# Optimization experiments

Measured on AMD Instinct MI355X. Metric: run time of the kernel, lower is better.

## Reference

```python
import jax, jax.numpy as jnp
import numpy as np

NUM_HEADS = 16

def setup_inputs() -> dict:
    key = jax.random.key(0)
    ks = jax.random.split(key, 6)
    B, S, D = 4, 2048, 1024
    sc = 1.0 / np.sqrt(D)
    return {
        "x": jax.random.normal(ks[0], (B, S, D), jnp.float32),
        "Wq": jax.random.normal(ks[1], (D, D), jnp.float32) * sc,
        "Wk": jax.random.normal(ks[2], (D, D), jnp.float32) * sc,
        "Wv": jax.random.normal(ks[3], (D, D), jnp.float32) * sc,
        "Wo": jax.random.normal(ks[4], (D, D), jnp.float32) * sc,
        "bo": jnp.zeros((D,), jnp.float32),
    }

def reference(x, Wq, Wk, Wv, Wo, bo):
    B, S, D = x.shape
    H = NUM_HEADS
    hd = D // H
    # projections (Linear: x @ W^T, but we store W as [d_in, d_out] so x @ W)
    q = (x @ Wq).reshape(B, S, H, hd)
    k = (x @ Wk).reshape(B, S, H, hd)
    v = (x @ Wv).reshape(B, S, H, hd)
    # scores: [B, H, S, S]
    scores = jnp.einsum("bqhd,bkhd->bhqk", q, k) / jnp.sqrt(jnp.asarray(hd, x.dtype))
    attn = jax.nn.softmax(scores, axis=-1)  # dropout p=0.0 (eval) -> identity
    ctx = jnp.einsum("bhqk,bkhd->bqhd", attn, v).reshape(B, S, D)
    return ctx @ Wo + bo
```

## Files before the change

kernel.cpp:

```cpp
#include <hip/hip_runtime.h>
#include <hip/hip_bf16.h>

typedef __bf16 bf16x8 __attribute__((ext_vector_type(8)));
typedef float f32x4 __attribute__((ext_vector_type(4)));

#define D_MODEL 1024
#define SEQ 2048
#define BATCH 4
#define HEADS 16
#define HD 64
#define M_TOT (BATCH * SEQ)
#define QPW 4

static __device__ __forceinline__ unsigned short f2bf(float f) {
  unsigned int u = __float_as_uint(f);
  unsigned int lsb = (u >> 16) & 1u;
  u += 0x7fffu + lsb;
  return (unsigned short)(u >> 16);
}

static __device__ __forceinline__ void glds16(const void* g, void* l) {
  __builtin_amdgcn_global_load_lds(
      (const __attribute__((address_space(1))) unsigned int*)g,
      (__attribute__((address_space(3))) unsigned int*)l, 16, 0, 0);
}

__global__ __launch_bounds__(256) void cvt_x_kernel(const float* __restrict__ x,
                                                    unsigned short* __restrict__ xb,
                                                    int n4) {
  int i = blockIdx.x * 256 + threadIdx.x;
  if (i >= n4) return;
  const float4 v = reinterpret_cast<const float4*>(x)[i];
  ushort4 o;
  o.x = f2bf(v.x); o.y = f2bf(v.y); o.z = f2bf(v.z); o.w = f2bf(v.w);
  reinterpret_cast<ushort4*>(xb)[i] = o;
}

__global__ __launch_bounds__(256) void transW_kernel(const float* __restrict__ W,
                                                     unsigned short* __restrict__ Wt) {
  __shared__ float t[32][33];
  int bx = blockIdx.x * 32;
  int by = blockIdx.y * 32;
  int tx = threadIdx.x, ty = threadIdx.y;
#pragma unroll
  for (int i = 0; i < 32; i += 8)
    t[ty + i][tx] = W[(size_t)(by + ty + i) * D_MODEL + bx + tx];
  __syncthreads();
#pragma unroll
  for (int i = 0; i < 32; i += 8)
    Wt[(size_t)(bx + ty + i) * D_MODEL + by + tx] = f2bf(t[tx][ty + i]);
}

template <int MODE>
__global__ __launch_bounds__(256) void gemm_bt_kernel(
    const unsigned short* __restrict__ A, const unsigned short* __restrict__ Bt,
    void* __restrict__ out, const float* __restrict__ bias, int M, int N, int K,
    float scale) {
  __shared__ __align__(16) unsigned short Als[128 * 64];
  __shared__ __align__(16) unsigned short Bls[128 * 64];

  const int tid = threadIdx.x;
  const int l = tid & 63;
  const int wave = tid >> 6;
  const int l15 = l & 15;
  const int lk = l >> 4;
  const int wm = wave >> 1, wn = wave & 1;

  const int nblocks_n = N >> 7;
  const int mblk = blockIdx.x / nblocks_n;
  const int nblk = blockIdx.x % nblocks_n;
  const int m0 = mblk << 7, n0 = nblk << 7;

  f32x4 acc[4][4] = {};

  const int srow0 = wave * 32 + (l >> 3);
  const int scolb = (l & 7) * 16;
  char* alsb = (char*)Als;
  char* blsb = (char*)Bls;

  for (int k0 = 0; k0 < K; k0 += 64) {
    __syncthreads();
#pragma unroll
    for (int j = 0; j < 4; ++j) {
      const int row = srow0 + j * 8;
      glds16((const char*)A + ((size_t)(m0 + row) * K + k0) * 2 + scolb,
             alsb + (wave * 32 + j * 8) * 128);
      glds16((const char*)Bt + ((size_t)(n0 + row) * K + k0) * 2 + scolb,
             blsb + (wave * 32 + j * 8) * 128);
    }
    __syncthreads();
#pragma unroll
    for (int kk = 0; kk < 2; ++kk) {
      bf16x8 af[4], bfr[4];
#pragma unroll
      for (int m = 0; m < 4; ++m)
        af[m] = *reinterpret_cast<const bf16x8*>(
            alsb + (wm * 64 + m * 16 + l15) * 128 + kk * 64 + lk * 16);
#pragma unroll
      for (int n = 0; n < 4; ++n)
        bfr[n] = *reinterpret_cast<const bf16x8*>(
            blsb + (wn * 64 + n * 16 + l15) * 128 + kk * 64 + lk * 16);
#pragma unroll
      for (int m = 0; m < 4; ++m)
#pragma unroll
        for (int n = 0; n < 4; ++n)
          acc[m][n] = __builtin_amdgcn_mfma_f32_16x16x32_bf16(af[m], bfr[n], acc[m][n], 0, 0, 0);
    }
  }

#pragma unroll
  for (int m = 0; m < 4; ++m) {
#pragma unroll
    for (int n = 0; n < 4; ++n) {
      const int row0 = wm * 64 + m * 16 + lk * 4;
      const int col = wn * 64 + n * 16 + l15;
      const int gm0 = m0 + row0;
      const int gn = n0 + col;
      if (MODE == 0) {
        unsigned short* o = (unsigned short*)out;
#pragma unroll
        for (int r = 0; r < 4; ++r)
          o[(size_t)(gm0 + r) * N + gn] = f2bf(acc[m][n][r] * scale);
      } else if (MODE == 1) {
        unsigned short* o = (unsigned short*)out;
        int b = gm0 >> 11, s = gm0 & 2047;
        int h = gn >> 6, d = gn & 63;
        size_t base = ((size_t)((b * HEADS + h) * HD + d)) * SEQ + s;
#pragma unroll
        for (int r = 0; r < 4; ++r) o[base + r] = f2bf(acc[m][n][r]);
      } else {
        float* o = (float*)out;
        float bv = bias[gn];
#pragma unroll
        for (int r = 0; r < 4; ++r)
          o[(size_t)(gm0 + r) * N + gn] = acc[m][n][r] + bv;
      }
    }
  }
}

__global__ __launch_bounds__(256) void attn_kernel(const unsigned short* __restrict__ Q,
                                                   const unsigned short* __restrict__ Kb,
                                                   const unsigned short* __restrict__ Vt,
                                                   unsigned short* __restrict__ ctx) {
  __shared__ __align__(16) unsigned short Kls[2][64 * 64];
  __shared__ __align__(16) unsigned short Vls[2][64 * 64];

  const int tid = threadIdx.x;
  const int l = tid & 63;
  const int wave = tid >> 6;
  const int l15 = l & 15;
  const int lk = l >> 4;

  const int bid = blockIdx.x;
  const int nid = (bid & 7) * 64 + (bid >> 3);
  const int qt = nid & 7;
  const int bh = nid >> 3;
  const int b = bh >> 4;
  const int h = bh & 15;

  const int qbase = b * SEQ + qt * 256 + wave * 64;

  bf16x8 qf[QPW][2];
#pragma unroll
  for (int qb = 0; qb < QPW; ++qb)
#pragma unroll
    for (int kk = 0; kk < 2; ++kk)
      qf[qb][kk] = *reinterpret_cast<const bf16x8*>(
          &Q[(size_t)(qbase + qb * 16 + l15) * D_MODEL + h * HD + kk * 32 + lk * 8]);

  f32x4 acc[QPW][4] = {};
  float lsum[QPW] = {};

  const int srow = tid >> 2;
  const int sc = tid & 3;
  const int krow = (srow & 32) | ((srow & 4) << 2) | ((srow >> 1) & 12) | (srow & 3);

  const size_t kgbase = ((size_t)b * SEQ) * D_MODEL + h * HD;
  const size_t vgbase = ((size_t)(b * HEADS + h) * HD) * SEQ;

  uint4 kreg[2], vreg[2];
#pragma unroll
  for (int i = 0; i < 2; ++i) {
    kreg[i] = *reinterpret_cast<const uint4*>(
        &Kb[kgbase + (size_t)srow * D_MODEL + sc * 8 + i * 32]);
    vreg[i] = *reinterpret_cast<const uint4*>(
        &Vt[vgbase + (size_t)srow * SEQ + sc * 8 + i * 32]);
  }

  int p = 0;
  for (int kt = 0; kt < SEQ / 64; ++kt) {
    char* klsb = (char*)Kls[p];
    char* vlsb = (char*)Vls[p];
#pragma unroll
    for (int i = 0; i < 2; ++i) {
      *reinterpret_cast<uint4*>(
          klsb + krow * 128 + ((sc * 16 + i * 64) ^ ((krow & 7) << 4))) = kreg[i];
      *reinterpret_cast<uint4*>(
          vlsb + srow * 128 + ((sc * 16 + i * 64) ^ ((srow & 7) << 4))) = vreg[i];
    }
    __syncthreads();

    if (kt + 1 < SEQ / 64) {
      const int nt = kt + 1;
#pragma unroll
      for (int i = 0; i < 2; ++i) {
        kreg[i] = *reinterpret_cast<const uint4*>(
            &Kb[kgbase + (size_t)(nt * 64 + srow) * D_MODEL + sc * 8 + i * 32]);
        vreg[i] = *reinterpret_cast<const uint4*>(
            &Vt[vgbase + (size_t)srow * SEQ + nt * 64 + sc * 8 + i * 32]);
      }
    }

    f32x4 s[QPW][4] = {};
#pragma unroll
    for (int kk = 0; kk < 2; ++kk) {
      bf16x8 kf[4];
#pragma unroll
      for (int n = 0; n < 4; ++n)
        kf[n] = *reinterpret_cast<const bf16x8*>(
            klsb + (n * 16 + l15) * 128 + ((kk * 64 + lk * 16) ^ ((l15 & 7) << 4)));
#pragma unroll
      for (int qb = 0; qb < QPW; ++qb)
#pragma unroll
        for (int n = 0; n < 4; ++n)
          s[qb][n] = __builtin_amdgcn_mfma_f32_16x16x32_bf16(kf[n], qf[qb][kk], s[qb][n], 0, 0, 0);
    }

    bf16x8 pvv[QPW][2];
#pragma unroll
    for (int qb = 0; qb < QPW; ++qb) {
      float ps = 0.f;
#pragma unroll
      for (int n = 0; n < 4; ++n)
#pragma unroll
        for (int r = 0; r < 4; ++r) {
          float pp = __builtin_amdgcn_exp2f(s[qb][n][r]);
          ps += pp;
          pvv[qb][n >> 1][(n & 1) * 4 + r] = (__bf16)pp;
        }
      lsum[qb] += ps;
    }

#pragma unroll
    for (int kk = 0; kk < 2; ++kk) {
      bf16x8 vf[4];
#pragma unroll
      for (int nd = 0; nd < 4; ++nd)
        vf[nd] = *reinterpret_cast<const bf16x8*>(
            vlsb + (nd * 16 + l15) * 128 + ((kk * 64 + lk * 16) ^ ((l15 & 7) << 4)));
#pragma unroll
      for (int qb = 0; qb < QPW; ++qb)
#pragma unroll
        for (int nd = 0; nd < 4; ++nd)
          acc[qb][nd] = __builtin_amdgcn_mfma_f32_16x16x32_bf16(vf[nd], pvv[qb][kk], acc[qb][nd], 0, 0, 0);
    }
    p ^= 1;
  }

#pragma unroll
  for (int qb = 0; qb < QPW; ++qb) {
    float t = lsum[qb];
    t += __shfl_xor(t, 16);
    t += __shfl_xor(t, 32);
    const float inv = 1.0f / t;
    const size_t row = (size_t)(qbase + qb * 16 + l15) * D_MODEL + h * HD;
#pragma unroll
    for (int nd = 0; nd < 4; ++nd) {
      ushort4 ov;
      ov.x = f2bf(acc[qb][nd][0] * inv);
      ov.y = f2bf(acc[qb][nd][1] * inv);
      ov.z = f2bf(acc[qb][nd][2] * inv);
      ov.w = f2bf(acc[qb][nd][3] * inv);
      *reinterpret_cast<ushort4*>(&ctx[row + nd * 16 + lk * 4]) = ov;
    }
  }
}

extern "C" void kernel_launch(void* const* d_in, const int* in_sizes, int n_in,
                              void* d_out, int out_size, void* d_ws, size_t ws_size,
                              hipStream_t stream) {
  const float* x = (const float*)d_in[0];
  const float* Wq = (const float*)d_in[1];
  const float* Wk = (const float*)d_in[2];
  const float* Wv = (const float*)d_in[3];
  const float* Wo = (const float*)d_in[4];
  const float* bo = (const float*)d_in[5];

  char* ws = (char*)d_ws;
  const size_t MB = 1u << 20;
  unsigned short* xb = (unsigned short*)(ws + 0 * MB);
  unsigned short* WqT = (unsigned short*)(ws + 16 * MB);
  unsigned short* WkT = (unsigned short*)(ws + 18 * MB);
  unsigned short* WvT = (unsigned short*)(ws + 20 * MB);
  unsigned short* WoT = (unsigned short*)(ws + 22 * MB);
  unsigned short* Qb = (unsigned short*)(ws + 24 * MB);
  unsigned short* Kb = (unsigned short*)(ws + 40 * MB);
  unsigned short* Vt = (unsigned short*)(ws + 56 * MB);
  unsigned short* ctx = (unsigned short*)(ws + 72 * MB);

  int n4 = (M_TOT * D_MODEL) / 4;
  cvt_x_kernel<<<n4 / 256, 256, 0, stream>>>(x, xb, n4);

  dim3 tb(32, 8);
  dim3 tg(32, 32);
  transW_kernel<<<tg, tb, 0, stream>>>(Wq, WqT);
  transW_kernel<<<tg, tb, 0, stream>>>(Wk, WkT);
  transW_kernel<<<tg, tb, 0, stream>>>(Wv, WvT);
  transW_kernel<<<tg, tb, 0, stream>>>(Wo, WoT);

  int gblocks = (M_TOT / 128) * (D_MODEL / 128);
  gemm_bt_kernel<0><<<gblocks, 256, 0, stream>>>(xb, WqT, Qb, nullptr, M_TOT, D_MODEL, D_MODEL,
                                                 0.125f * 1.44269504f);
  gemm_bt_kernel<0><<<gblocks, 256, 0, stream>>>(xb, WkT, Kb, nullptr, M_TOT, D_MODEL, D_MODEL, 1.0f);
  gemm_bt_kernel<1><<<gblocks, 256, 0, stream>>>(xb, WvT, Vt, nullptr, M_TOT, D_MODEL, D_MODEL, 1.0f);

  attn_kernel<<<BATCH * HEADS * (SEQ / 256), 256, 0, stream>>>(Qb, Kb, Vt, ctx);

  gemm_bt_kernel<2><<<gblocks, 256, 0, stream>>>(ctx, WoT, d_out, bo, M_TOT, D_MODEL, D_MODEL, 1.0f);
}
```

Measured before the change: 247.8 us.

## Double-buffer GEMM LDS tiles and raise wave priority around MFMA blocks

```diff
diff --git a/kernel.cpp b/kernel.cpp
--- a/kernel.cpp
+++ b/kernel.cpp
@@ -56,8 +56,8 @@
     const unsigned short* __restrict__ A, const unsigned short* __restrict__ Bt,
     void* __restrict__ out, const float* __restrict__ bias, int M, int N, int K,
     float scale) {
-  __shared__ __align__(16) unsigned short Als[128 * 64];
-  __shared__ __align__(16) unsigned short Bls[128 * 64];
+  __shared__ __align__(16) unsigned short Als[2][128 * 64];
+  __shared__ __align__(16) unsigned short Bls[2][128 * 64];
 
   const int tid = threadIdx.x;
   const int l = tid & 63;
@@ -75,20 +75,31 @@
 
   const int srow0 = wave * 32 + (l >> 3);
   const int scolb = (l & 7) * 16;
-  char* alsb = (char*)Als;
-  char* blsb = (char*)Bls;
-
+
+#pragma unroll
+  for (int j = 0; j < 4; ++j) {
+    const int row = srow0 + j * 8;
+    glds16((const char*)A + ((size_t)(m0 + row) * K) * 2 + scolb,
+           (char*)Als[0] + (wave * 32 + j * 8) * 128);
+    glds16((const char*)Bt + ((size_t)(n0 + row) * K) * 2 + scolb,
+           (char*)Bls[0] + (wave * 32 + j * 8) * 128);
+  }
+  __syncthreads();
+
+  int p = 0;
   for (int k0 = 0; k0 < K; k0 += 64) {
-    __syncthreads();
-#pragma unroll
-    for (int j = 0; j < 4; ++j) {
-      const int row = srow0 + j * 8;
-      glds16((const char*)A + ((size_t)(m0 + row) * K + k0) * 2 + scolb,
-             alsb + (wave * 32 + j * 8) * 128);
-      glds16((const char*)Bt + ((size_t)(n0 + row) * K + k0) * 2 + scolb,
-             blsb + (wave * 32 + j * 8) * 128);
-    }
-    __syncthreads();
+    if (k0 + 64 < K) {
+#pragma unroll
+      for (int j = 0; j < 4; ++j) {
+        const int row = srow0 + j * 8;
+        glds16((const char*)A + ((size_t)(m0 + row) * K + k0 + 64) * 2 + scolb,
+               (char*)Als[p ^ 1] + (wave * 32 + j * 8) * 128);
+        glds16((const char*)Bt + ((size_t)(n0 + row) * K + k0 + 64) * 2 + scolb,
+               (char*)Bls[p ^ 1] + (wave * 32 + j * 8) * 128);
+      }
+    }
+    const char* alsb = (const char*)Als[p];
+    const char* blsb = (const char*)Bls[p];
 #pragma unroll
     for (int kk = 0; kk < 2; ++kk) {
       bf16x8 af[4], bfr[4];
@@ -100,12 +111,16 @@
       for (int n = 0; n < 4; ++n)
         bfr[n] = *reinterpret_cast<const bf16x8*>(
             blsb + (wn * 64 + n * 16 + l15) * 128 + kk * 64 + lk * 16);
+      __builtin_amdgcn_s_setprio(1);
 #pragma unroll
       for (int m = 0; m < 4; ++m)
 #pragma unroll
         for (int n = 0; n < 4; ++n)
           acc[m][n] = __builtin_amdgcn_mfma_f32_16x16x32_bf16(af[m], bfr[n], acc[m][n], 0, 0, 0);
-    }
+      __builtin_amdgcn_s_setprio(0);
+    }
+    __syncthreads();
+    p ^= 1;
   }
 
 #pragma unroll
@@ -220,11 +235,13 @@
       for (int n = 0; n < 4; ++n)
         kf[n] = *reinterpret_cast<const bf16x8*>(
             klsb + (n * 16 + l15) * 128 + ((kk * 64 + lk * 16) ^ ((l15 & 7) << 4)));
+      __builtin_amdgcn_s_setprio(1);
 #pragma unroll
       for (int qb = 0; qb < QPW; ++qb)
 #pragma unroll
         for (int n = 0; n < 4; ++n)
           s[qb][n] = __builtin_amdgcn_mfma_f32_16x16x32_bf16(kf[n], qf[qb][kk], s[qb][n], 0, 0, 0);
+      __builtin_amdgcn_s_setprio(0);
     }
 
     bf16x8 pvv[QPW][2];
@@ -249,11 +266,13 @@
       for (int nd = 0; nd < 4; ++nd)
         vf[nd] = *reinterpret_cast<const bf16x8*>(
             vlsb + (nd * 16 + l15) * 128 + ((kk * 64 + lk * 16) ^ ((l15 & 7) << 4)));
+      __builtin_amdgcn_s_setprio(1);
 #pragma unroll
       for (int qb = 0; qb < QPW; ++qb)
 #pragma unroll
         for (int nd = 0; nd < 4; ++nd)
           acc[qb][nd] = __builtin_amdgcn_mfma_f32_16x16x32_bf16(vf[nd], pvv[qb][kk], acc[qb][nd], 0, 0, 0);
+      __builtin_amdgcn_s_setprio(0);
     }
     p ^= 1;
   }
```

New measurement: 269.0 us. 8.6% more time.
